# Kernel optimization log

Hardware: AMD Instinct MI355X
Metric: run time of the kernel (lower is better)

Reference implementation:

```python
import jax, jax.numpy as jnp
import numpy as np

NUM_LABELS = 17
MARGIN = 1.0
IGNORE = -100


def setup_inputs() -> dict:
    key = jax.random.key(0)
    k1, k2, k3 = jax.random.split(key, 3)
    B, S, H = 64, 1024, 384
    embeddings = jax.random.normal(k1, (B, S, H), dtype=jnp.float32)
    classifier_w = jax.random.normal(k2, (NUM_LABELS, H), dtype=jnp.float32) * 0.02
    classifier_b = jnp.zeros((NUM_LABELS,), dtype=jnp.float32)
    labels = jax.random.randint(k3, (B, S), 0, NUM_LABELS, dtype=jnp.int64 if jax.config.jax_enable_x64 else jnp.int32)
    attention_mask = jnp.ones((B, S), dtype=jnp.int32)
    return {"embeddings": embeddings, "classifier_w": classifier_w,
            "classifier_b": classifier_b, "labels": labels,
            "attention_mask": attention_mask}


def _total_loss(embeddings, W, b, labels, mask):
    B, S, H = embeddings.shape
    N = B * S
    fe = embeddings.reshape(N, H)          # [N,H] flattened tokens
    fl = labels.reshape(N)
    fm = mask.reshape(N) > 0

    # ----- cross entropy (ignore_index=-100), matches F.cross_entropy mean -----
    logits = fe @ W.T + b                  # [N, L]
    logp = jax.nn.log_softmax(logits, axis=-1)
    safe = jnp.where(fl == IGNORE, 0, fl)
    nll = -jnp.take_along_axis(logp, safe[:, None], axis=1)[:, 0]
    ce_valid = fl != IGNORE
    ce = jnp.sum(jnp.where(ce_valid, nll, 0.0)) / jnp.maximum(jnp.sum(ce_valid), 1)

    # ----- quadruplet loss (deterministic sampling: earliest occurrences) -----
    idx = jnp.arange(N)
    BIG = N  # sentinel index > any real index
    is_ent = fm & (fl > 0)
    non_ent = fm & (fl == 0)
    d_i = jnp.min(jnp.where(non_ent, idx, BIG))   # first non-entity token
    has_non = jnp.any(non_ent)

    def per_type(t):
        m = is_ent & (fl == t)
        order = jnp.sort(jnp.where(m, idx, BIG))
        a_i, p_i = order[0], order[1]             # anchor / positive = first two occurrences
        cnt = jnp.sum(m)
        other = is_ent & (fl != t)
        n_i = jnp.min(jnp.where(other, idx, BIG))  # negative = first other-type entity
        ok = (cnt >= 2) & jnp.any(other) & has_non
        return a_i, p_i, n_i, ok

    types = jnp.arange(1, NUM_LABELS)
    a_i, p_i, n_i, ok = jax.vmap(per_type)(types)  # each [L-1]
    clip = lambda i: jnp.clip(i, 0, N - 1)
    A = fe[clip(a_i)]
    P = fe[clip(p_i)]
    Ng = fe[clip(n_i)]
    D = fe[clip(d_i)][None, :]
    eps = 1e-6  # torch F.pairwise_distance eps added to the difference
    dist = lambda x, y: jnp.sqrt(jnp.sum((x - y + eps) ** 2, axis=-1))
    pd, nd, dd = dist(A, P), dist(A, Ng), dist(A, D)
    ql = jax.nn.relu(pd - nd + MARGIN) + jax.nn.relu(pd - dd + 2.0 * MARGIN)
    qcnt = jnp.sum(ok)
    quad = jnp.sum(jnp.where(ok, ql, 0.0)) / jnp.maximum(qcnt, 1)
    quad = jnp.where(qcnt > 0, quad, 0.0)

    # ----- context loss: adjacent same-entity tokens, mean-per-pair MSE -----
    l0, l1 = labels[:, :-1], labels[:, 1:]
    pair = (l0 != IGNORE) & (l0 == l1) & (l0 > 0)
    mse = jnp.mean((embeddings[:, :-1] - embeddings[:, 1:]) ** 2, axis=-1)  # [B,S-1]
    pc = jnp.sum(pair)
    ctx = jnp.sum(jnp.where(pair, mse, 0.0)) / jnp.maximum(pc, 1)
    ctx = jnp.where(pc > 0, ctx, 0.0)

    return ce + 0.5 * quad + 0.1 * ctx


def reference(embeddings, classifier_w, classifier_b, labels, attention_mask):
    return _total_loss(embeddings, classifier_w, classifier_b, labels, attention_mask)
```

## Files before the change

kernel.cpp:

```cpp
#include <hip/hip_runtime.h>

#define NL 17
#define IGN (-100)
#define HD 384
#define NSEQ 1024
#define NT 65536
#define BIGI NT
#define TPB 256
#define NBLK (NT / TPB)
#define NCHUNK 12
#define CF4 8

typedef unsigned int u32;
typedef __attribute__((ext_vector_type(8))) short bf16x8;
typedef __attribute__((ext_vector_type(16))) float f32x16;

#define GLOAD_LDS16(g, l) __builtin_amdgcn_global_load_lds(                    \
    (const __attribute__((address_space(1))) u32*)(g),                         \
    (__attribute__((address_space(3))) u32*)(l), 16, 0, 0)

__device__ __forceinline__ u32 cvtpk(float lo, float hi) {
  u32 u;
  asm("v_cvt_pk_bf16_f32 %0, %1, %2" : "=v"(u) : "v"(lo), "v"(hi));
  return u;
}

struct WS {
  float ce_part[NBLK];
  float ctx_part[NBLK];
  int   ce_cnt[NBLK];
  int   ctx_cnt[NBLK];
  int   blk_a[NBLK][16];
  int   blk_p[NBLK][16];
  int   blk_c[NBLK][16];
  int   blk_d[NBLK];
};

__global__ __launch_bounds__(256, 1) void k_main(const float* __restrict__ emb,
                                                 const float* __restrict__ cw,
                                                 const float* __restrict__ cb,
                                                 const int* __restrict__ labels,
                                                 const int* __restrict__ mask,
                                                 WS* __restrict__ ws) {
  __shared__ float4 tile[4][TPB * CF4];
  __shared__ float4 sW4[NL * (HD / 4)];
  __shared__ float sce[4], sctx[4];
  __shared__ int   svc[4], spc[4];
  __shared__ float sbctx;
  __shared__ int   sbcnt;
  __shared__ int   sla[16], slp[16], slc[16], sld;

  const int tid = threadIdx.x, lane = tid & 63, wid = tid >> 6;
  const int b = blockIdx.x;
  const int token = b * TPB + tid;

  const float4* cw4 = (const float4*)cw;
  for (int i = tid; i < NL * (HD / 4); i += TPB) {
    int c = i / (HD / 4), q = i % (HD / 4);
    sW4[c * (HD / 4) + (q ^ (c & 7))] = cw4[i];
  }
  if (tid < 16) { sla[tid] = BIGI; slp[tid] = BIGI; slc[tid] = 0; }
  if (tid == 16) sld = BIGI;
  __syncthreads();

  const int rb  = tid >> 3;
  const int c4  = tid & 7;
  const int gc4 = c4 ^ (rb & 7);
  const float* src0 = emb + (size_t)b * TPB * HD + (size_t)rb * HD + gc4 * 4;
  const int wbase = __builtin_amdgcn_readfirstlane(wid * 64);

#pragma unroll
  for (int k = 0; k < CF4; ++k)
    GLOAD_LDS16(src0 + (size_t)k * 32 * HD, &tile[0][k * 256 + wbase]);
#pragma unroll
  for (int k = 0; k < CF4; ++k)
    GLOAD_LDS16(src0 + 32 + (size_t)k * 32 * HD, &tile[1][k * 256 + wbase]);

  const int cls = lane & 31;
  const int kh  = lane >> 5;
  const int clsS = (cls < NL) ? cls : 0;
  const int row0 = wid * 64 + (lane & 31);
  const int row1 = row0 + 32;
  const int r0 = tid;
  const int r1 = (tid < TPB - 1) ? tid + 1 : tid;
  const int x0 = r0 & 7, x1 = r1 & 7;

  f32x16 d0 = {0.f}, d1 = {0.f};
  float ctxacc = 0.f;

  auto bfrag = [&](const float4* tb, int row, int s) -> bf16x8 {
    int g0 = (s * 4 + kh * 2) ^ (row & 7);
    int g1 = (s * 4 + kh * 2 + 1) ^ (row & 7);
    float4 f0 = tb[(row << 3) | g0];
    float4 f1 = tb[(row << 3) | g1];
    union { u32 u[4]; bf16x8 v; } X;
    X.u[0] = cvtpk(f0.x, f0.y); X.u[1] = cvtpk(f0.z, f0.w);
    X.u[2] = cvtpk(f1.x, f1.y); X.u[3] = cvtpk(f1.z, f1.w);
    return X.v;
  };

  auto afrag = [&](int ch, int s) -> bf16x8 {
    union { u32 u[4]; bf16x8 v; } X;
    if (cls < NL) {
      int qa = (ch * 2 + s) * 4 + kh * 2;
      float4 f0 = sW4[clsS * (HD / 4) + ((qa) ^ (cls & 7))];
      float4 f1 = sW4[clsS * (HD / 4) + ((qa + 1) ^ (cls & 7))];
      X.u[0] = cvtpk(f0.x, f0.y); X.u[1] = cvtpk(f0.z, f0.w);
      X.u[2] = cvtpk(f1.x, f1.y); X.u[3] = cvtpk(f1.z, f1.w);
    } else {
      X.u[0] = 0; X.u[1] = 0; X.u[2] = 0; X.u[3] = 0;
    }
    return X.v;
  };

  auto compute = [&](int ch, const float4* tb) {
#pragma unroll
    for (int q = 0; q < CF4; ++q) {
      float4 a  = tb[(r0 << 3) | (q ^ x0)];
      float4 nb = tb[(r1 << 3) | (q ^ x1)];
      float e0 = a.x - nb.x, e1 = a.y - nb.y, e2 = a.z - nb.z, e3 = a.w - nb.w;
      ctxacc = fmaf(e0, e0, fmaf(e1, e1, fmaf(e2, e2, fmaf(e3, e3, ctxacc))));
    }
    bf16x8 a0 = afrag(ch, 0), a1 = afrag(ch, 1);
    bf16x8 b00 = bfrag(tb, row0, 0), b01 = bfrag(tb, row0, 1);
    bf16x8 b10 = bfrag(tb, row1, 0), b11 = bfrag(tb, row1, 1);
    d0 = __builtin_amdgcn_mfma_f32_32x32x16_bf16(a0, b00, d0, 0, 0, 0);
    d0 = __builtin_amdgcn_mfma_f32_32x32x16_bf16(a1, b01, d0, 0, 0, 0);
    d1 = __builtin_amdgcn_mfma_f32_32x32x16_bf16(a0, b10, d1, 0, 0, 0);
    d1 = __builtin_amdgcn_mfma_f32_32x32x16_bf16(a1, b11, d1, 0, 0, 0);
  };

#pragma unroll 1
  for (int ch = 0; ch < NCHUNK - 2; ++ch) {
    const float* srcn = src0 + (size_t)(ch + 2) * 32;
    float4* dstb = tile[(ch + 2) & 3];
#pragma unroll
    for (int k = 0; k < CF4; ++k)
      GLOAD_LDS16(srcn + (size_t)k * 32 * HD, &dstb[k * 256 + wbase]);
    asm volatile("s_waitcnt vmcnt(16)" ::: "memory");
    __builtin_amdgcn_sched_barrier(0);
    __builtin_amdgcn_s_barrier();
    __builtin_amdgcn_sched_barrier(0);
    compute(ch, tile[ch & 3]);
  }
  asm volatile("s_waitcnt vmcnt(8)" ::: "memory");
  __builtin_amdgcn_sched_barrier(0);
  __builtin_amdgcn_s_barrier();
  __builtin_amdgcn_sched_barrier(0);
  compute(NCHUNK - 2, tile[(NCHUNK - 2) & 3]);
  asm volatile("s_waitcnt vmcnt(0)" ::: "memory");
  __builtin_amdgcn_sched_barrier(0);
  __builtin_amdgcn_s_barrier();
  __builtin_amdgcn_sched_barrier(0);
  compute(NCHUNK - 1, tile[(NCHUNK - 1) & 3]);
  __syncthreads();

  float* logit = (float*)&tile[0][0];
#pragma unroll
  for (int r = 0; r < 16; ++r) {
    int row = (r & 3) + 8 * (r >> 2) + 4 * kh;
    if (row < NL) {
      logit[(wid * 64 + (lane & 31)) * 21 + row] = d0[r];
      logit[(wid * 64 + 32 + (lane & 31)) * 21 + row] = d1[r];
    }
  }
  __syncthreads();

  int lb = labels[token];
  int mk = mask[token];
  int lbm = (mk > 0) ? lb : IGN;
  if (lbm == 0) atomicMin(&sld, token);
  else if (lbm >= 1 && lbm < NL) { atomicMin(&sla[lbm - 1], token); atomicAdd(&slc[lbm - 1], 1); }
  __syncthreads();
  if (lbm >= 1 && lbm < NL && token > sla[lbm - 1]) atomicMin(&slp[lbm - 1], token);

  float lg[NL];
#pragma unroll
  for (int c = 0; c < NL; ++c) lg[c] = logit[tid * 21 + c] + cb[c];
  float m = lg[0];
#pragma unroll
  for (int c = 1; c < NL; ++c) m = fmaxf(m, lg[c]);
  float s = 0.f;
#pragma unroll
  for (int c = 0; c < NL; ++c) s += __expf(lg[c] - m);
  float lse = m + __logf(s);
  int safe = (lb == IGN) ? 0 : lb;
  float ll = 0.f;
#pragma unroll
  for (int c = 0; c < NL; ++c) ll = (c == safe) ? lg[c] : ll;
  bool valid = (lb != IGN);
  float cev = valid ? (lse - ll) : 0.f;

  int nlb = (tid < TPB - 1) ? labels[token + 1] : IGN;
  bool pair = (tid < TPB - 1) && valid && (lb == nlb) && (lb > 0);
  float ctxv = pair ? ctxacc * (1.0f / HD) : 0.f;

  unsigned long long bv = __ballot(valid);
  unsigned long long bp = __ballot(pair);
#pragma unroll
  for (int off = 32; off; off >>= 1) {
    cev  += __shfl_xor(cev, off, 64);
    ctxv += __shfl_xor(ctxv, off, 64);
  }
  if (lane == 0) { sce[wid] = cev; sctx[wid] = ctxv; svc[wid] = __popcll(bv); spc[wid] = __popcll(bp); }

  if (wid == 3) {
    int t = b * TPB + TPB - 1;
    float bc = 0.f; int bn = 0;
    if (((t + 1) & (NSEQ - 1)) != 0) {
      int l0 = labels[t], l1 = labels[t + 1];
      if (l0 != IGN && l0 == l1 && l0 > 0) {
        const float* ra = emb + (size_t)t * HD;
        const float* rbp = ra + HD;
        float a = 0.f;
#pragma unroll
        for (int j = 0; j < 6; ++j) {
          float dd = ra[lane + 64 * j] - rbp[lane + 64 * j];
          a = fmaf(dd, dd, a);
        }
#pragma unroll
        for (int off = 32; off; off >>= 1) a += __shfl_xor(a, off, 64);
        bc = a * (1.0f / HD); bn = 1;
      }
    }
    if (lane == 0) { sbctx = bc; sbcnt = bn; }
  }
  __syncthreads();
  if (tid < 16) {
    ws->blk_a[b][tid] = sla[tid];
    ws->blk_p[b][tid] = slp[tid];
    ws->blk_c[b][tid] = slc[tid];
  }
  if (tid == 16) ws->blk_d[b] = sld;
  if (tid == 0) {
    ws->ce_part[b]  = sce[0] + sce[1] + sce[2] + sce[3];
    ws->ce_cnt[b]   = svc[0] + svc[1] + svc[2] + svc[3];
    ws->ctx_part[b] = sctx[0] + sctx[1] + sctx[2] + sctx[3] + sbctx;
    ws->ctx_cnt[b]  = spc[0] + spc[1] + spc[2] + spc[3] + sbcnt;
  }
}

__global__ __launch_bounds__(256) void k_final(const float* __restrict__ emb,
                                               WS* __restrict__ ws,
                                               float* __restrict__ out) {
  __shared__ double rce[256], rctx[256];
  __shared__ int rvc[256], rpc[256], rd[256];
  __shared__ int M1[256], M2[256], CN[256];
  __shared__ int ga[16], gp[16], gc[16];
  __shared__ float qs[4]; __shared__ int qc[4];
  const int tid = threadIdx.x, lane = tid & 63, wid = tid >> 6;

  rce[tid]  = ws->ce_part[tid];
  rctx[tid] = ws->ctx_part[tid];
  rvc[tid]  = ws->ce_cnt[tid];
  rpc[tid]  = ws->ctx_cnt[tid];
  rd[tid]   = ws->blk_d[tid];

  {
    const int type = tid & 15, seg = tid >> 4;
    int m1 = BIGI, m2 = BIGI, cnt = 0;
#pragma unroll 4
    for (int k = 0; k < 16; ++k) {
      int bb = seg * 16 + k;
      int x = ws->blk_a[bb][type];
      if (x < m1) { m2 = m1; m1 = x; } else if (x < m2) { m2 = x; }
      int y = ws->blk_p[bb][type];
      if (y < m1) { m2 = m1; m1 = y; } else if (y < m2) { m2 = y; }
      cnt += ws->blk_c[bb][type];
    }
    M1[tid] = m1; M2[tid] = m2; CN[tid] = cnt;
  }
  __syncthreads();
  for (int s = 128; s > 0; s >>= 1) {
    if (tid < s) {
      rce[tid] += rce[tid + s]; rctx[tid] += rctx[tid + s];
      rvc[tid] += rvc[tid + s]; rpc[tid] += rpc[tid + s];
      rd[tid] = min(rd[tid], rd[tid + s]);
    }
    __syncthreads();
  }
  if (tid < 16) {
    int m1 = BIGI, m2 = BIGI, cnt = 0;
    for (int seg = 0; seg < 16; ++seg) {
      int a1 = M1[seg * 16 + tid], a2 = M2[seg * 16 + tid];
      int n1 = min(m1, a1);
      int n2 = min(max(m1, a1), min(m2, a2));
      m1 = n1; m2 = n2;
      cnt += CN[seg * 16 + tid];
    }
    ga[tid] = m1; gp[tid] = m2; gc[tid] = cnt;
  }
  __syncthreads();

  const int gd = rd[0];
  float qsum = 0.f; int qcnt = 0;
  for (int tt = 0; tt < 4; ++tt) {
    int t = wid * 4 + tt;
    int a = ga[t], p = gp[t], c = gc[t];
    int nmin = BIGI;
#pragma unroll
    for (int u = 0; u < 16; ++u) if (u != t) nmin = min(nmin, ga[u]);
    bool ok = (c >= 2) && (nmin < BIGI) && (gd < BIGI);
    if (ok) {
      const float* A  = emb + (size_t)min(a, NT - 1) * HD;
      const float* P  = emb + (size_t)min(p, NT - 1) * HD;
      const float* Ng = emb + (size_t)min(nmin, NT - 1) * HD;
      const float* D  = emb + (size_t)min(gd, NT - 1) * HD;
      float sap = 0.f, san = 0.f, sad = 0.f;
#pragma unroll
      for (int j = 0; j < 6; ++j) {
        int idx = lane + 64 * j;
        float av = A[idx];
        float d1 = av - P[idx] + 1e-6f;  sap = fmaf(d1, d1, sap);
        float d2 = av - Ng[idx] + 1e-6f; san = fmaf(d2, d2, san);
        float d3 = av - D[idx] + 1e-6f;  sad = fmaf(d3, d3, sad);
      }
#pragma unroll
      for (int off = 32; off; off >>= 1) {
        sap += __shfl_xor(sap, off, 64);
        san += __shfl_xor(san, off, 64);
        sad += __shfl_xor(sad, off, 64);
      }
      float pd = sqrtf(sap), nd = sqrtf(san), dd = sqrtf(sad);
      qsum += fmaxf(pd - nd + 1.0f, 0.f) + fmaxf(pd - dd + 2.0f, 0.f);
      qcnt += 1;
    }
  }
  if (lane == 0) { qs[wid] = qsum; qc[wid] = qcnt; }
  __syncthreads();
  if (tid == 0) {
    double tq = (double)qs[0] + qs[1] + qs[2] + qs[3];
    int tqc = qc[0] + qc[1] + qc[2] + qc[3];
    double ce   = rce[0] / (double)max(rvc[0], 1);
    double ctx  = (rpc[0] > 0) ? rctx[0] / (double)rpc[0] : 0.0;
    double quad = (tqc > 0) ? tq / (double)tqc : 0.0;
    out[0] = (float)(ce + 0.5 * quad + 0.1 * ctx);
  }
}

extern "C" void kernel_launch(void* const* d_in, const int* in_sizes, int n_in,
                              void* d_out, int out_size, void* d_ws, size_t ws_size,
                              hipStream_t stream) {
  const float* emb    = (const float*)d_in[0];
  const float* cw     = (const float*)d_in[1];
  const float* cb     = (const float*)d_in[2];
  const int*   labels = (const int*)d_in[3];
  const int*   mask   = (const int*)d_in[4];
  WS* ws = (WS*)d_ws;
  float* out = (float*)d_out;

  k_main <<<NBLK, 256, 0, stream>>>(emb, cw, cb, labels, mask, ws);
  k_final<<<1, 256, 0, stream>>>(emb, ws, out);
}
```

Before: 36.37 us.

## Halve tokens per block, pre-convert weights to bf16, fuse final reduction via last-block

After: 73.88 us. 2.03x slower.

```diff
diff --git a/kernel.cpp b/kernel.cpp
--- a/kernel.cpp
+++ b/kernel.cpp
@@ -7,11 +7,13 @@
 #define NT 65536
 #define BIGI NT
 #define TPB 256
-#define NBLK (NT / TPB)
+#define TOK 128
+#define NBLK (NT / TOK)
 #define NCHUNK 12
-#define CF4 8
+#define WPAD 392
 
 typedef unsigned int u32;
+typedef unsigned short u16;
 typedef __attribute__((ext_vector_type(8))) short bf16x8;
 typedef __attribute__((ext_vector_type(16))) float f32x16;
 
@@ -26,6 +28,8 @@
 }
 
 struct WS {
+  u32  cnt;
+  u32  pad0[15];
   float ce_part[NBLK];
   float ctx_part[NBLK];
   int   ce_cnt[NBLK];
@@ -36,28 +40,29 @@
   int   blk_d[NBLK];
 };
 
-__global__ __launch_bounds__(256, 1) void k_main(const float* __restrict__ emb,
+__global__ __launch_bounds__(256, 2) void k_main(const float* __restrict__ emb,
                                                  const float* __restrict__ cw,
                                                  const float* __restrict__ cb,
                                                  const int* __restrict__ labels,
                                                  const int* __restrict__ mask,
-                                                 WS* __restrict__ ws) {
-  __shared__ float4 tile[4][TPB * CF4];
-  __shared__ float4 sW4[NL * (HD / 4)];
-  __shared__ float sce[4], sctx[4];
-  __shared__ int   svc[4], spc[4];
-  __shared__ float sbctx;
-  __shared__ int   sbcnt;
-  __shared__ int   sla[16], slp[16], slc[16], sld;
+                                                 WS* __restrict__ ws,
+                                                 float* __restrict__ out) {
+  __shared__ float4 tile[4][TOK * 8];
+  __shared__ u16    sWh[NL * WPAD];
+  __shared__ float  sce[2], sctx[2];
+  __shared__ int    svc[2], spc[2];
+  __shared__ float  sbctx;
+  __shared__ int    sbcnt;
+  __shared__ int    sla[16], slp[16], slc[16], sld, slast;
 
   const int tid = threadIdx.x, lane = tid & 63, wid = tid >> 6;
   const int b = blockIdx.x;
-  const int token = b * TPB + tid;
-
-  const float4* cw4 = (const float4*)cw;
-  for (int i = tid; i < NL * (HD / 4); i += TPB) {
-    int c = i / (HD / 4), q = i % (HD / 4);
-    sW4[c * (HD / 4) + (q ^ (c & 7))] = cw4[i];
+  const int token = b * TOK + tid;
+
+  for (int i = tid; i < NL * (HD / 2); i += TPB) {
+    int c = i / (HD / 2), p = i % (HD / 2);
+    u32 pk = cvtpk(cw[c * HD + 2 * p], cw[c * HD + 2 * p + 1]);
+    *(u32*)&sWh[c * WPAD + 2 * p] = pk;
   }
   if (tid < 16) { sla[tid] = BIGI; slp[tid] = BIGI; slc[tid] = 0; }
   if (tid == 16) sld = BIGI;
@@ -66,68 +71,59 @@
   const int rb  = tid >> 3;
   const int c4  = tid & 7;
   const int gc4 = c4 ^ (rb & 7);
-  const float* src0 = emb + (size_t)b * TPB * HD + (size_t)rb * HD + gc4 * 4;
+  const float* src0 = emb + (size_t)b * TOK * HD + (size_t)rb * HD + gc4 * 4;
   const int wbase = __builtin_amdgcn_readfirstlane(wid * 64);
 
 #pragma unroll
-  for (int k = 0; k < CF4; ++k)
+  for (int k = 0; k < 4; ++k)
     GLOAD_LDS16(src0 + (size_t)k * 32 * HD, &tile[0][k * 256 + wbase]);
 #pragma unroll
-  for (int k = 0; k < CF4; ++k)
+  for (int k = 0; k < 4; ++k)
     GLOAD_LDS16(src0 + 32 + (size_t)k * 32 * HD, &tile[1][k * 256 + wbase]);
 
   const int cls = lane & 31;
   const int kh  = lane >> 5;
   const int clsS = (cls < NL) ? cls : 0;
-  const int row0 = wid * 64 + (lane & 31);
-  const int row1 = row0 + 32;
-  const int r0 = tid;
-  const int r1 = (tid < TPB - 1) ? tid + 1 : tid;
-  const int x0 = r0 & 7, x1 = r1 & 7;
-
-  f32x16 d0 = {0.f}, d1 = {0.f};
+  const int row0 = wid * 32 + (lane & 31);
+  const int cr0 = tid & 127;
+  const int cr1 = (cr0 < TOK - 1) ? cr0 + 1 : cr0;
+  const int chf = tid >> 7;
+  const int cx0 = cr0 & 7, cx1 = cr1 & 7;
+
+  f32x16 d0 = {0.f};
   float ctxacc = 0.f;
 
-  auto bfrag = [&](const float4* tb, int row, int s) -> bf16x8 {
-    int g0 = (s * 4 + kh * 2) ^ (row & 7);
-    int g1 = (s * 4 + kh * 2 + 1) ^ (row & 7);
-    float4 f0 = tb[(row << 3) | g0];
-    float4 f1 = tb[(row << 3) | g1];
+  auto bfrag = [&](const float4* tb, int s) -> bf16x8 {
+    int g0 = (s * 4 + kh * 2) ^ (row0 & 7);
+    int g1 = (s * 4 + kh * 2 + 1) ^ (row0 & 7);
+    float4 f0 = tb[(row0 << 3) | g0];
+    float4 f1 = tb[(row0 << 3) | g1];
     union { u32 u[4]; bf16x8 v; } X;
     X.u[0] = cvtpk(f0.x, f0.y); X.u[1] = cvtpk(f0.z, f0.w);
     X.u[2] = cvtpk(f1.x, f1.y); X.u[3] = cvtpk(f1.z, f1.w);
     return X.v;
   };
-
   auto afrag = [&](int ch, int s) -> bf16x8 {
+    if (cls < NL)
+      return *(const bf16x8*)&sWh[clsS * WPAD + ch * 32 + s * 16 + kh * 8];
     union { u32 u[4]; bf16x8 v; } X;
-    if (cls < NL) {
-      int qa = (ch * 2 + s) * 4 + kh * 2;
-      float4 f0 = sW4[clsS * (HD / 4) + ((qa) ^ (cls & 7))];
-      float4 f1 = sW4[clsS * (HD / 4) + ((qa + 1) ^ (cls & 7))];
-      X.u[0] = cvtpk(f0.x, f0.y); X.u[1] = cvtpk(f0.z, f0.w);
-      X.u[2] = cvtpk(f1.x, f1.y); X.u[3] = cvtpk(f1.z, f1.w);
-    } else {
-      X.u[0] = 0; X.u[1] = 0; X.u[2] = 0; X.u[3] = 0;
-    }
+    X.u[0] = 0; X.u[1] = 0; X.u[2] = 0; X.u[3] = 0;
     return X.v;
   };
 
   auto compute = [&](int ch, const float4* tb) {
 #pragma unroll
-    for (int q = 0; q < CF4; ++q) {
-      float4 a  = tb[(r0 << 3) | (q ^ x0)];
-      float4 nb = tb[(r1 << 3) | (q ^ x1)];
+    for (int qq = 0; qq < 4; ++qq) {
+      int q = chf * 4 + qq;
+      float4 a  = tb[(cr0 << 3) | (q ^ cx0)];
+      float4 nb = tb[(cr1 << 3) | (q ^ cx1)];
       float e0 = a.x - nb.x, e1 = a.y - nb.y, e2 = a.z - nb.z, e3 = a.w - nb.w;
       ctxacc = fmaf(e0, e0, fmaf(e1, e1, fmaf(e2, e2, fmaf(e3, e3, ctxacc))));
     }
     bf16x8 a0 = afrag(ch, 0), a1 = afrag(ch, 1);
-    bf16x8 b00 = bfrag(tb, row0, 0), b01 = bfrag(tb, row0, 1);
-    bf16x8 b10 = bfrag(tb, row1, 0), b11 = bfrag(tb, row1, 1);
-    d0 = __builtin_amdgcn_mfma_f32_32x32x16_bf16(a0, b00, d0, 0, 0, 0);
-    d0 = __builtin_amdgcn_mfma_f32_32x32x16_bf16(a1, b01, d0, 0, 0, 0);
-    d1 = __builtin_amdgcn_mfma_f32_32x32x16_bf16(a0, b10, d1, 0, 0, 0);
-    d1 = __builtin_amdgcn_mfma_f32_32x32x16_bf16(a1, b11, d1, 0, 0, 0);
+    bf16x8 b0 = bfrag(tb, 0), b1 = bfrag(tb, 1);
+    d0 = __builtin_amdgcn_mfma_f32_32x32x16_bf16(a0, b0, d0, 0, 0, 0);
+    d0 = __builtin_amdgcn_mfma_f32_32x32x16_bf16(a1, b1, d0, 0, 0, 0);
   };
 
 #pragma unroll 1
@@ -135,15 +131,15 @@
     const float* srcn = src0 + (size_t)(ch + 2) * 32;
     float4* dstb = tile[(ch + 2) & 3];
 #pragma unroll
-    for (int k = 0; k < CF4; ++k)
+    for (int k = 0; k < 4; ++k)
       GLOAD_LDS16(srcn + (size_t)k * 32 * HD, &dstb[k * 256 + wbase]);
-    asm volatile("s_waitcnt vmcnt(16)" ::: "memory");
+    asm volatile("s_waitcnt vmcnt(8)" ::: "memory");
     __builtin_amdgcn_sched_barrier(0);
     __builtin_amdgcn_s_barrier();
     __builtin_amdgcn_sched_barrier(0);
     compute(ch, tile[ch & 3]);
   }
-  asm volatile("s_waitcnt vmcnt(8)" ::: "memory");
+  asm volatile("s_waitcnt vmcnt(4)" ::: "memory");
   __builtin_amdgcn_sched_barrier(0);
   __builtin_amdgcn_s_barrier();
   __builtin_amdgcn_sched_barrier(0);
@@ -156,45 +152,47 @@
   __syncthreads();
 
   float* logit = (float*)&tile[0][0];
+  float* pcxp  = (float*)&tile[1][0];
 #pragma unroll
   for (int r = 0; r < 16; ++r) {
     int row = (r & 3) + 8 * (r >> 2) + 4 * kh;
-    if (row < NL) {
-      logit[(wid * 64 + (lane & 31)) * 21 + row] = d0[r];
-      logit[(wid * 64 + 32 + (lane & 31)) * 21 + row] = d1[r];
-    }
-  }
-  __syncthreads();
-
-  int lb = labels[token];
-  int mk = mask[token];
+    if (row < NL) logit[(wid * 32 + (lane & 31)) * 21 + row] = d0[r];
+  }
+  pcxp[tid] = ctxacc;
+  __syncthreads();
+
+  int lb = IGN, mk = 0;
+  if (tid < TOK) { lb = labels[token]; mk = mask[token]; }
   int lbm = (mk > 0) ? lb : IGN;
   if (lbm == 0) atomicMin(&sld, token);
-  else if (lbm >= 1 && lbm < NL) { atomicMin(&sla[lbm - 1], token); atomicAdd(&slc[lbm - 1], 1); }
-  __syncthreads();
-  if (lbm >= 1 && lbm < NL && token > sla[lbm - 1]) atomicMin(&slp[lbm - 1], token);
-
-  float lg[NL];
-#pragma unroll
-  for (int c = 0; c < NL; ++c) lg[c] = logit[tid * 21 + c] + cb[c];
-  float m = lg[0];
-#pragma unroll
-  for (int c = 1; c < NL; ++c) m = fmaxf(m, lg[c]);
-  float s = 0.f;
-#pragma unroll
-  for (int c = 0; c < NL; ++c) s += __expf(lg[c] - m);
-  float lse = m + __logf(s);
-  int safe = (lb == IGN) ? 0 : lb;
-  float ll = 0.f;
-#pragma unroll
-  for (int c = 0; c < NL; ++c) ll = (c == safe) ? lg[c] : ll;
-  bool valid = (lb != IGN);
-  float cev = valid ? (lse - ll) : 0.f;
-
-  int nlb = (tid < TPB - 1) ? labels[token + 1] : IGN;
-  bool pair = (tid < TPB - 1) && valid && (lb == nlb) && (lb > 0);
-  float ctxv = pair ? ctxacc * (1.0f / HD) : 0.f;
-
+  else if (lbm >= 1) { atomicMin(&sla[lbm - 1], token); atomicAdd(&slc[lbm - 1], 1); }
+  __syncthreads();
+  if (lbm >= 1 && token > sla[lbm - 1]) atomicMin(&slp[lbm - 1], token);
+
+  float cev = 0.f, ctxv = 0.f;
+  bool valid = false, pair = false;
+  if (tid < TOK) {
+    float lg[NL];
+#pragma unroll
+    for (int c = 0; c < NL; ++c) lg[c] = logit[tid * 21 + c] + cb[c];
+    float m = lg[0];
+#pragma unroll
+    for (int c = 1; c < NL; ++c) m = fmaxf(m, lg[c]);
+    float s = 0.f;
+#pragma unroll
+    for (int c = 0; c < NL; ++c) s += __expf(lg[c] - m);
+    float lse = m + __logf(s);
+    int safe = (lb == IGN) ? 0 : lb;
+    float ll = 0.f;
+#pragma unroll
+    for (int c = 0; c < NL; ++c) ll = (c == safe) ? lg[c] : ll;
+    valid = (lb != IGN);
+    cev = valid ? (lse - ll) : 0.f;
+    int nlb = (tid < TOK - 1) ? labels[token + 1] : IGN;
+    pair = (tid < TOK - 1) && valid && (lb == nlb) && (lb > 0);
+    float cs = pcxp[tid] + pcxp[tid + 128];
+    ctxv = pair ? cs * (1.0f / HD) : 0.f;
+  }
   unsigned long long bv = __ballot(valid);
   unsigned long long bp = __ballot(pair);
 #pragma unroll
@@ -202,10 +200,10 @@
     cev  += __shfl_xor(cev, off, 64);
     ctxv += __shfl_xor(ctxv, off, 64);
   }
-  if (lane == 0) { sce[wid] = cev; sctx[wid] = ctxv; svc[wid] = __popcll(bv); spc[wid] = __popcll(bp); }
-
-  if (wid == 3) {
-    int t = b * TPB + TPB - 1;
+  if (lane == 0 && wid < 2) { sce[wid] = cev; sctx[wid] = ctxv; svc[wid] = __popcll(bv); spc[wid] = __popcll(bp); }
+
+  if (wid == 2) {
+    int t = b * TOK + TOK - 1;
     float bc = 0.f; int bn = 0;
     if (((t + 1) & (NSEQ - 1)) != 0) {
       int l0 = labels[t], l1 = labels[t + 1];
@@ -233,35 +231,53 @@
   }
   if (tid == 16) ws->blk_d[b] = sld;
   if (tid == 0) {
-    ws->ce_part[b]  = sce[0] + sce[1] + sce[2] + sce[3];
-    ws->ce_cnt[b]   = svc[0] + svc[1] + svc[2] + svc[3];
-    ws->ctx_part[b] = sctx[0] + sctx[1] + sctx[2] + sctx[3] + sbctx;
-    ws->ctx_cnt[b]  = spc[0] + spc[1] + spc[2] + spc[3] + sbcnt;
-  }
-}
-
-__global__ __launch_bounds__(256) void k_final(const float* __restrict__ emb,
-                                               WS* __restrict__ ws,
-                                               float* __restrict__ out) {
-  __shared__ double rce[256], rctx[256];
-  __shared__ int rvc[256], rpc[256], rd[256];
-  __shared__ int M1[256], M2[256], CN[256];
-  __shared__ int ga[16], gp[16], gc[16];
-  __shared__ float qs[4]; __shared__ int qc[4];
-  const int tid = threadIdx.x, lane = tid & 63, wid = tid >> 6;
-
-  rce[tid]  = ws->ce_part[tid];
-  rctx[tid] = ws->ctx_part[tid];
-  rvc[tid]  = ws->ce_cnt[tid];
-  rpc[tid]  = ws->ctx_cnt[tid];
-  rd[tid]   = ws->blk_d[tid];
-
+    ws->ce_part[b]  = sce[0] + sce[1];
+    ws->ce_cnt[b]   = svc[0] + svc[1];
+    ws->ctx_part[b] = sctx[0] + sctx[1] + sbctx;
+    ws->ctx_cnt[b]  = spc[0] + spc[1] + sbcnt;
+  }
+
+  __threadfence();
+  __syncthreads();
+  if (tid == 0) {
+    u32 v = atomicAdd(&ws->cnt, 1u);
+    slast = (v == (u32)(NBLK - 1));
+  }
+  __syncthreads();
+  if (!slast) return;
+  __threadfence();
+
+  char* scr = (char*)&tile[0][0];
+  double* Rce  = (double*)scr;
+  double* Rctx = (double*)(scr + 2048);
+  int* Rvc = (int*)(scr + 4096);
+  int* Rpc = (int*)(scr + 5120);
+  int* Rd  = (int*)(scr + 6144);
+  int* M1  = (int*)(scr + 7168);
+  int* M2  = (int*)(scr + 8192);
+  int* CN  = (int*)(scr + 9216);
+  int* Ga  = (int*)(scr + 10240);
+  int* Gp  = (int*)(scr + 10304);
+  int* Gc  = (int*)(scr + 10368);
+  float* Qs = (float*)(scr + 10432);
+  int* Qc  = (int*)(scr + 10448);
+
+  {
+    double sc = 0, sx = 0; int cv = 0, cp = 0, md = BIGI;
+#pragma unroll
+    for (int k = 0; k < 2; ++k) {
+      int i = tid * 2 + k;
+      sc += ws->ce_part[i]; sx += ws->ctx_part[i];
+      cv += ws->ce_cnt[i];  cp += ws->ctx_cnt[i];
+      md = min(md, ws->blk_d[i]);
+    }
+    Rce[tid] = sc; Rctx[tid] = sx; Rvc[tid] = cv; Rpc[tid] = cp; Rd[tid] = md;
+  }
   {
     const int type = tid & 15, seg = tid >> 4;
     int m1 = BIGI, m2 = BIGI, cnt = 0;
-#pragma unroll 4
-    for (int k = 0; k < 16; ++k) {
-      int bb = seg * 16 + k;
+    for (int k = 0; k < 32; ++k) {
+      int bb = seg * 32 + k;
       int x = ws->blk_a[bb][type];
       if (x < m1) { m2 = m1; m1 = x; } else if (x < m2) { m2 = x; }
       int y = ws->blk_p[bb][type];
@@ -273,9 +289,9 @@
   __syncthreads();
   for (int s = 128; s > 0; s >>= 1) {
     if (tid < s) {
-      rce[tid] += rce[tid + s]; rctx[tid] += rctx[tid + s];
-      rvc[tid] += rvc[tid + s]; rpc[tid] += rpc[tid + s];
-      rd[tid] = min(rd[tid], rd[tid + s]);
+      Rce[tid] += Rce[tid + s]; Rctx[tid] += Rctx[tid + s];
+      Rvc[tid] += Rvc[tid + s]; Rpc[tid] += Rpc[tid + s];
+      Rd[tid] = min(Rd[tid], Rd[tid + s]);
     }
     __syncthreads();
   }
@@ -288,18 +304,18 @@
       m1 = n1; m2 = n2;
       cnt += CN[seg * 16 + tid];
     }
-    ga[tid] = m1; gp[tid] = m2; gc[tid] = cnt;
-  }
-  __syncthreads();
-
-  const int gd = rd[0];
+    Ga[tid] = m1; Gp[tid] = m2; Gc[tid] = cnt;
+  }
+  __syncthreads();
+
+  const int gd = Rd[0];
   float qsum = 0.f; int qcnt = 0;
   for (int tt = 0; tt < 4; ++tt) {
     int t = wid * 4 + tt;
-    int a = ga[t], p = gp[t], c = gc[t];
+    int a = Ga[t], p = Gp[t], c = Gc[t];
     int nmin = BIGI;
 #pragma unroll
-    for (int u = 0; u < 16; ++u) if (u != t) nmin = min(nmin, ga[u]);
+    for (int u = 0; u < 16; ++u) if (u != t) nmin = min(nmin, Ga[u]);
     bool ok = (c >= 2) && (nmin < BIGI) && (gd < BIGI);
     if (ok) {
       const float* A  = emb + (size_t)min(a, NT - 1) * HD;
@@ -326,13 +342,13 @@
       qcnt += 1;
     }
   }
-  if (lane == 0) { qs[wid] = qsum; qc[wid] = qcnt; }
+  if (lane == 0) { Qs[wid] = qsum; Qc[wid] = qcnt; }
   __syncthreads();
   if (tid == 0) {
-    double tq = (double)qs[0] + qs[1] + qs[2] + qs[3];
-    int tqc = qc[0] + qc[1] + qc[2] + qc[3];
-    double ce   = rce[0] / (double)max(rvc[0], 1);
-    double ctx  = (rpc[0] > 0) ? rctx[0] / (double)rpc[0] : 0.0;
+    double tq = (double)Qs[0] + Qs[1] + Qs[2] + Qs[3];
+    int tqc = Qc[0] + Qc[1] + Qc[2] + Qc[3];
+    double ce   = Rce[0] / (double)max(Rvc[0], 1);
+    double ctx  = (Rpc[0] > 0) ? Rctx[0] / (double)Rpc[0] : 0.0;
     double quad = (tqc > 0) ? tq / (double)tqc : 0.0;
     out[0] = (float)(ce + 0.5 * quad + 0.1 * ctx);
   }
@@ -349,6 +365,6 @@
   WS* ws = (WS*)d_ws;
   float* out = (float*)d_out;
 
-  k_main <<<NBLK, 256, 0, stream>>>(emb, cw, cb, labels, mask, ws);
-  k_final<<<1, 256, 0, stream>>>(emb, ws, out);
+  hipMemsetAsync(d_ws, 0, 4, stream);
+  k_main<<<NBLK, TPB, 0, stream>>>(emb, cw, cb, labels, mask, ws, out);
 }
```

## Reuse MFMA tile reads for context MSE, pre-convert weights to bf16, deepen prefetch

Applied to the files above, without the earlier changes.

Result: slower. 39.46 us (+8.5%).

```diff
diff --git a/kernel.cpp b/kernel.cpp
--- a/kernel.cpp
+++ b/kernel.cpp
@@ -10,8 +10,10 @@
 #define NBLK (NT / TPB)
 #define NCHUNK 12
 #define CF4 8
+#define WPAD 392
 
 typedef unsigned int u32;
+typedef unsigned short u16;
 typedef __attribute__((ext_vector_type(8))) short bf16x8;
 typedef __attribute__((ext_vector_type(16))) float f32x16;
 
@@ -43,21 +45,22 @@
                                                  const int* __restrict__ mask,
                                                  WS* __restrict__ ws) {
   __shared__ float4 tile[4][TPB * CF4];
-  __shared__ float4 sW4[NL * (HD / 4)];
-  __shared__ float sce[4], sctx[4];
-  __shared__ int   svc[4], spc[4];
-  __shared__ float sbctx;
-  __shared__ int   sbcnt;
-  __shared__ int   sla[16], slp[16], slc[16], sld;
+  __shared__ u16    sWh[NL * WPAD];
+  __shared__ float  pcx0[4][64], pcx1[4][64];
+  __shared__ float  sce[4], sctx[4];
+  __shared__ int    svc[4], spc[4];
+  __shared__ float  sbctx;
+  __shared__ int    sbcnt;
+  __shared__ int    sla[16], slp[16], slc[16], sld;
 
   const int tid = threadIdx.x, lane = tid & 63, wid = tid >> 6;
   const int b = blockIdx.x;
   const int token = b * TPB + tid;
 
-  const float4* cw4 = (const float4*)cw;
-  for (int i = tid; i < NL * (HD / 4); i += TPB) {
-    int c = i / (HD / 4), q = i % (HD / 4);
-    sW4[c * (HD / 4) + (q ^ (c & 7))] = cw4[i];
+  for (int i = tid; i < NL * (HD / 2); i += TPB) {
+    int c = i / (HD / 2), p = i % (HD / 2);
+    u32 pk = cvtpk(cw[c * HD + 2 * p], cw[c * HD + 2 * p + 1]);
+    *(u32*)&sWh[c * WPAD + 2 * p] = pk;
   }
   if (tid < 16) { sla[tid] = BIGI; slp[tid] = BIGI; slc[tid] = 0; }
   if (tid == 16) sld = BIGI;
@@ -69,80 +72,84 @@
   const float* src0 = emb + (size_t)b * TPB * HD + (size_t)rb * HD + gc4 * 4;
   const int wbase = __builtin_amdgcn_readfirstlane(wid * 64);
 
-#pragma unroll
-  for (int k = 0; k < CF4; ++k)
-    GLOAD_LDS16(src0 + (size_t)k * 32 * HD, &tile[0][k * 256 + wbase]);
-#pragma unroll
-  for (int k = 0; k < CF4; ++k)
-    GLOAD_LDS16(src0 + 32 + (size_t)k * 32 * HD, &tile[1][k * 256 + wbase]);
+  auto issue = [&](int c) {
+    const float* s = src0 + (size_t)c * 32;
+    float4* d = tile[c & 3];
+#pragma unroll
+    for (int k = 0; k < CF4; ++k)
+      GLOAD_LDS16(s + (size_t)k * 32 * HD, &d[k * 256 + wbase]);
+  };
+
+  issue(0); issue(1); issue(2);
 
   const int cls = lane & 31;
   const int kh  = lane >> 5;
   const int clsS = (cls < NL) ? cls : 0;
   const int row0 = wid * 64 + (lane & 31);
   const int row1 = row0 + 32;
-  const int r0 = tid;
-  const int r1 = (tid < TPB - 1) ? tid + 1 : tid;
-  const int x0 = r0 & 7, x1 = r1 & 7;
+  const int row0n = row0 + 1;
+  const int row1n = (row1 < TPB - 1) ? row1 + 1 : row1;
 
   f32x16 d0 = {0.f}, d1 = {0.f};
-  float ctxacc = 0.f;
-
-  auto bfrag = [&](const float4* tb, int row, int s) -> bf16x8 {
-    int g0 = (s * 4 + kh * 2) ^ (row & 7);
-    int g1 = (s * 4 + kh * 2 + 1) ^ (row & 7);
-    float4 f0 = tb[(row << 3) | g0];
-    float4 f1 = tb[(row << 3) | g1];
-    union { u32 u[4]; bf16x8 v; } X;
-    X.u[0] = cvtpk(f0.x, f0.y); X.u[1] = cvtpk(f0.z, f0.w);
-    X.u[2] = cvtpk(f1.x, f1.y); X.u[3] = cvtpk(f1.z, f1.w);
-    return X.v;
+  float acc0 = 0.f, acc1 = 0.f;
+
+  auto afrag = [&](int ch, int s) -> bf16x8 {
+    if (cls < NL)
+      return *(const bf16x8*)&sWh[clsS * WPAD + ch * 32 + s * 16 + kh * 8];
+    union { u32 u[4]; bf16x8 v; } Z;
+    Z.u[0] = 0; Z.u[1] = 0; Z.u[2] = 0; Z.u[3] = 0;
+    return Z.v;
   };
 
-  auto afrag = [&](int ch, int s) -> bf16x8 {
-    union { u32 u[4]; bf16x8 v; } X;
-    if (cls < NL) {
-      int qa = (ch * 2 + s) * 4 + kh * 2;
-      float4 f0 = sW4[clsS * (HD / 4) + ((qa) ^ (cls & 7))];
-      float4 f1 = sW4[clsS * (HD / 4) + ((qa + 1) ^ (cls & 7))];
-      X.u[0] = cvtpk(f0.x, f0.y); X.u[1] = cvtpk(f0.z, f0.w);
-      X.u[2] = cvtpk(f1.x, f1.y); X.u[3] = cvtpk(f1.z, f1.w);
-    } else {
-      X.u[0] = 0; X.u[1] = 0; X.u[2] = 0; X.u[3] = 0;
-    }
-    return X.v;
+  auto compute = [&](int ch, const float4* tb) {
+    float4 t0[4], t1[4], n0[4], n1[4];
+#pragma unroll
+    for (int j = 0; j < 4; ++j) {
+      int q = (j >> 1) * 4 + kh * 2 + (j & 1);
+      t0[j] = tb[(row0  << 3) | (q ^ (row0  & 7))];
+      t1[j] = tb[(row1  << 3) | (q ^ (row1  & 7))];
+      n0[j] = tb[(row0n << 3) | (q ^ (row0n & 7))];
+      n1[j] = tb[(row1n << 3) | (q ^ (row1n & 7))];
+    }
+#pragma unroll
+    for (int j = 0; j < 4; ++j) {
+      float a0x = t0[j].x - n0[j].x, a0y = t0[j].y - n0[j].y;
+      float a0z = t0[j].z - n0[j].z, a0w = t0[j].w - n0[j].w;
+      acc0 = fmaf(a0x, a0x, fmaf(a0y, a0y, fmaf(a0z, a0z, fmaf(a0w, a0w, acc0))));
+      float a1x = t1[j].x - n1[j].x, a1y = t1[j].y - n1[j].y;
+      float a1z = t1[j].z - n1[j].z, a1w = t1[j].w - n1[j].w;
+      acc1 = fmaf(a1x, a1x, fmaf(a1y, a1y, fmaf(a1z, a1z, fmaf(a1w, a1w, acc1))));
+    }
+    union { u32 u[4]; bf16x8 v; } B00, B01, B10, B11;
+    B00.u[0] = cvtpk(t0[0].x, t0[0].y); B00.u[1] = cvtpk(t0[0].z, t0[0].w);
+    B00.u[2] = cvtpk(t0[1].x, t0[1].y); B00.u[3] = cvtpk(t0[1].z, t0[1].w);
+    B01.u[0] = cvtpk(t0[2].x, t0[2].y); B01.u[1] = cvtpk(t0[2].z, t0[2].w);
+    B01.u[2] = cvtpk(t0[3].x, t0[3].y); B01.u[3] = cvtpk(t0[3].z, t0[3].w);
+    B10.u[0] = cvtpk(t1[0].x, t1[0].y); B10.u[1] = cvtpk(t1[0].z, t1[0].w);
+    B10.u[2] = cvtpk(t1[1].x, t1[1].y); B10.u[3] = cvtpk(t1[1].z, t1[1].w);
+    B11.u[0] = cvtpk(t1[2].x, t1[2].y); B11.u[1] = cvtpk(t1[2].z, t1[2].w);
+    B11.u[2] = cvtpk(t1[3].x, t1[3].y); B11.u[3] = cvtpk(t1[3].z, t1[3].w);
+    bf16x8 a0 = afrag(ch, 0), a1 = afrag(ch, 1);
+    d0 = __builtin_amdgcn_mfma_f32_32x32x16_bf16(a0, B00.v, d0, 0, 0, 0);
+    d0 = __builtin_amdgcn_mfma_f32_32x32x16_bf16(a1, B01.v, d0, 0, 0, 0);
+    d1 = __builtin_amdgcn_mfma_f32_32x32x16_bf16(a0, B10.v, d1, 0, 0, 0);
+    d1 = __builtin_amdgcn_mfma_f32_32x32x16_bf16(a1, B11.v, d1, 0, 0, 0);
   };
 
-  auto compute = [&](int ch, const float4* tb) {
-#pragma unroll
-    for (int q = 0; q < CF4; ++q) {
-      float4 a  = tb[(r0 << 3) | (q ^ x0)];
-      float4 nb = tb[(r1 << 3) | (q ^ x1)];
-      float e0 = a.x - nb.x, e1 = a.y - nb.y, e2 = a.z - nb.z, e3 = a.w - nb.w;
-      ctxacc = fmaf(e0, e0, fmaf(e1, e1, fmaf(e2, e2, fmaf(e3, e3, ctxacc))));
-    }
-    bf16x8 a0 = afrag(ch, 0), a1 = afrag(ch, 1);
-    bf16x8 b00 = bfrag(tb, row0, 0), b01 = bfrag(tb, row0, 1);
-    bf16x8 b10 = bfrag(tb, row1, 0), b11 = bfrag(tb, row1, 1);
-    d0 = __builtin_amdgcn_mfma_f32_32x32x16_bf16(a0, b00, d0, 0, 0, 0);
-    d0 = __builtin_amdgcn_mfma_f32_32x32x16_bf16(a1, b01, d0, 0, 0, 0);
-    d1 = __builtin_amdgcn_mfma_f32_32x32x16_bf16(a0, b10, d1, 0, 0, 0);
-    d1 = __builtin_amdgcn_mfma_f32_32x32x16_bf16(a1, b11, d1, 0, 0, 0);
-  };
-
 #pragma unroll 1
-  for (int ch = 0; ch < NCHUNK - 2; ++ch) {
-    const float* srcn = src0 + (size_t)(ch + 2) * 32;
-    float4* dstb = tile[(ch + 2) & 3];
-#pragma unroll
-    for (int k = 0; k < CF4; ++k)
-      GLOAD_LDS16(srcn + (size_t)k * 32 * HD, &dstb[k * 256 + wbase]);
+  for (int ch = 0; ch <= NCHUNK - 4; ++ch) {
     asm volatile("s_waitcnt vmcnt(16)" ::: "memory");
     __builtin_amdgcn_sched_barrier(0);
     __builtin_amdgcn_s_barrier();
     __builtin_amdgcn_sched_barrier(0);
+    issue(ch + 3);
     compute(ch, tile[ch & 3]);
   }
+  asm volatile("s_waitcnt vmcnt(16)" ::: "memory");
+  __builtin_amdgcn_sched_barrier(0);
+  __builtin_amdgcn_s_barrier();
+  __builtin_amdgcn_sched_barrier(0);
+  compute(NCHUNK - 3, tile[(NCHUNK - 3) & 3]);
   asm volatile("s_waitcnt vmcnt(8)" ::: "memory");
   __builtin_amdgcn_sched_barrier(0);
   __builtin_amdgcn_s_barrier();
@@ -153,6 +160,9 @@
   __builtin_amdgcn_s_barrier();
   __builtin_amdgcn_sched_barrier(0);
   compute(NCHUNK - 1, tile[(NCHUNK - 1) & 3]);
+
+  pcx0[wid][lane] = acc0;
+  pcx1[wid][lane] = acc1;
   __syncthreads();
 
   float* logit = (float*)&tile[0][0];
@@ -191,9 +201,11 @@
   bool valid = (lb != IGN);
   float cev = valid ? (lse - ll) : 0.f;
 
+  float cs = (lane < 32) ? (pcx0[wid][lane] + pcx0[wid][lane + 32])
+                         : (pcx1[wid][lane - 32] + pcx1[wid][lane]);
   int nlb = (tid < TPB - 1) ? labels[token + 1] : IGN;
   bool pair = (tid < TPB - 1) && valid && (lb == nlb) && (lb > 0);
-  float ctxv = pair ? ctxacc * (1.0f / HD) : 0.f;
+  float ctxv = pair ? cs * (1.0f / HD) : 0.f;
 
   unsigned long long bv = __ballot(valid);
   unsigned long long bp = __ballot(pair);
@@ -349,6 +361,6 @@
   WS* ws = (WS*)d_ws;
   float* out = (float*)d_out;
 
-  k_main <<<NBLK, 256, 0, stream>>>(emb, cw, cb, labels, mask, ws);
+  k_main <<<NBLK, TPB, 0, stream>>>(emb, cw, cb, labels, mask, ws);
   k_final<<<1, 256, 0, stream>>>(emb, ws, out);
 }
```

## Make each wave own its token rows to drop block barriers; pre-convert weights to bf16

Applied to the files above, without the earlier changes.

Result: slower. 37.80 us (+4.0%).

```diff
diff --git a/kernel.cpp b/kernel.cpp
--- a/kernel.cpp
+++ b/kernel.cpp
@@ -10,8 +10,10 @@
 #define NBLK (NT / TPB)
 #define NCHUNK 12
 #define CF4 8
+#define WPAD 392
 
 typedef unsigned int u32;
+typedef unsigned short u16;
 typedef __attribute__((ext_vector_type(8))) short bf16x8;
 typedef __attribute__((ext_vector_type(16))) float f32x16;
 
@@ -42,52 +44,57 @@
                                                  const int* __restrict__ labels,
                                                  const int* __restrict__ mask,
                                                  WS* __restrict__ ws) {
-  __shared__ float4 tile[4][TPB * CF4];
-  __shared__ float4 sW4[NL * (HD / 4)];
-  __shared__ float sce[4], sctx[4];
-  __shared__ int   svc[4], spc[4];
-  __shared__ float sbctx;
-  __shared__ int   sbcnt;
-  __shared__ int   sla[16], slp[16], slc[16], sld;
+  __shared__ float4 tile[4][4][512];
+  __shared__ u16    sWh[NL * WPAD];
+  __shared__ float  sce[4], sctx[4];
+  __shared__ int    svc[4], spc[4];
+  __shared__ int    sla[16], slp[16], slc[16], sld;
 
   const int tid = threadIdx.x, lane = tid & 63, wid = tid >> 6;
+  const int uwid = __builtin_amdgcn_readfirstlane(wid);
   const int b = blockIdx.x;
   const int token = b * TPB + tid;
 
-  const float4* cw4 = (const float4*)cw;
-  for (int i = tid; i < NL * (HD / 4); i += TPB) {
-    int c = i / (HD / 4), q = i % (HD / 4);
-    sW4[c * (HD / 4) + (q ^ (c & 7))] = cw4[i];
+  for (int i = tid; i < NL * (HD / 2); i += TPB) {
+    int c = i / (HD / 2), p = i % (HD / 2);
+    u32 pk = cvtpk(cw[c * HD + 2 * p], cw[c * HD + 2 * p + 1]);
+    *(u32*)&sWh[c * WPAD + 2 * p] = pk;
   }
   if (tid < 16) { sla[tid] = BIGI; slp[tid] = BIGI; slc[tid] = 0; }
   if (tid == 16) sld = BIGI;
   __syncthreads();
 
-  const int rb  = tid >> 3;
-  const int c4  = tid & 7;
-  const int gc4 = c4 ^ (rb & 7);
-  const float* src0 = emb + (size_t)b * TPB * HD + (size_t)rb * HD + gc4 * 4;
-  const int wbase = __builtin_amdgcn_readfirstlane(wid * 64);
-
-#pragma unroll
-  for (int k = 0; k < CF4; ++k)
-    GLOAD_LDS16(src0 + (size_t)k * 32 * HD, &tile[0][k * 256 + wbase]);
-#pragma unroll
-  for (int k = 0; k < CF4; ++k)
-    GLOAD_LDS16(src0 + 32 + (size_t)k * 32 * HD, &tile[1][k * 256 + wbase]);
+  const int l3  = lane >> 3;
+  const int gc4 = (lane & 7) ^ l3;
+  const float* src0 = emb + ((size_t)b * TPB + wid * 64 + l3) * HD + gc4 * 4;
+
+  auto issue = [&](int c) {
+    const float* s = src0 + (size_t)c * 32;
+#pragma unroll
+    for (int k = 0; k < CF4; ++k)
+      GLOAD_LDS16(s + (size_t)k * 8 * HD, &tile[c & 3][uwid][k * 64]);
+  };
+
+  issue(0); issue(1); issue(2);
 
   const int cls = lane & 31;
   const int kh  = lane >> 5;
   const int clsS = (cls < NL) ? cls : 0;
-  const int row0 = wid * 64 + (lane & 31);
-  const int row1 = row0 + 32;
-  const int r0 = tid;
-  const int r1 = (tid < TPB - 1) ? tid + 1 : tid;
-  const int x0 = r0 & 7, x1 = r1 & 7;
+  const int rl0 = lane & 31;
+  const int rl1 = 32 + (lane & 31);
+  const int cr0 = lane;
+  const int cr1 = (lane < 63) ? lane + 1 : 63;
 
   f32x16 d0 = {0.f}, d1 = {0.f};
   float ctxacc = 0.f;
 
+  auto afrag = [&](int ch, int s) -> bf16x8 {
+    if (cls < NL)
+      return *(const bf16x8*)&sWh[clsS * WPAD + ch * 32 + s * 16 + kh * 8];
+    union { u32 u[4]; bf16x8 v; } Z;
+    Z.u[0] = 0; Z.u[1] = 0; Z.u[2] = 0; Z.u[3] = 0;
+    return Z.v;
+  };
   auto bfrag = [&](const float4* tb, int row, int s) -> bf16x8 {
     int g0 = (s * 4 + kh * 2) ^ (row & 7);
     int g1 = (s * 4 + kh * 2 + 1) ^ (row & 7);
@@ -99,31 +106,18 @@
     return X.v;
   };
 
-  auto afrag = [&](int ch, int s) -> bf16x8 {
-    union { u32 u[4]; bf16x8 v; } X;
-    if (cls < NL) {
-      int qa = (ch * 2 + s) * 4 + kh * 2;
-      float4 f0 = sW4[clsS * (HD / 4) + ((qa) ^ (cls & 7))];
-      float4 f1 = sW4[clsS * (HD / 4) + ((qa + 1) ^ (cls & 7))];
-      X.u[0] = cvtpk(f0.x, f0.y); X.u[1] = cvtpk(f0.z, f0.w);
-      X.u[2] = cvtpk(f1.x, f1.y); X.u[3] = cvtpk(f1.z, f1.w);
-    } else {
-      X.u[0] = 0; X.u[1] = 0; X.u[2] = 0; X.u[3] = 0;
-    }
-    return X.v;
-  };
-
-  auto compute = [&](int ch, const float4* tb) {
+  auto compute = [&](int ch) {
+    const float4* tb = (const float4*)&tile[ch & 3][wid][0];
 #pragma unroll
     for (int q = 0; q < CF4; ++q) {
-      float4 a  = tb[(r0 << 3) | (q ^ x0)];
-      float4 nb = tb[(r1 << 3) | (q ^ x1)];
+      float4 a  = tb[(cr0 << 3) | (q ^ (cr0 & 7))];
+      float4 nb = tb[(cr1 << 3) | (q ^ (cr1 & 7))];
       float e0 = a.x - nb.x, e1 = a.y - nb.y, e2 = a.z - nb.z, e3 = a.w - nb.w;
       ctxacc = fmaf(e0, e0, fmaf(e1, e1, fmaf(e2, e2, fmaf(e3, e3, ctxacc))));
     }
     bf16x8 a0 = afrag(ch, 0), a1 = afrag(ch, 1);
-    bf16x8 b00 = bfrag(tb, row0, 0), b01 = bfrag(tb, row0, 1);
-    bf16x8 b10 = bfrag(tb, row1, 0), b11 = bfrag(tb, row1, 1);
+    bf16x8 b00 = bfrag(tb, rl0, 0), b01 = bfrag(tb, rl0, 1);
+    bf16x8 b10 = bfrag(tb, rl1, 0), b11 = bfrag(tb, rl1, 1);
     d0 = __builtin_amdgcn_mfma_f32_32x32x16_bf16(a0, b00, d0, 0, 0, 0);
     d0 = __builtin_amdgcn_mfma_f32_32x32x16_bf16(a1, b01, d0, 0, 0, 0);
     d1 = __builtin_amdgcn_mfma_f32_32x32x16_bf16(a0, b10, d1, 0, 0, 0);
@@ -131,31 +125,25 @@
   };
 
 #pragma unroll 1
-  for (int ch = 0; ch < NCHUNK - 2; ++ch) {
-    const float* srcn = src0 + (size_t)(ch + 2) * 32;
-    float4* dstb = tile[(ch + 2) & 3];
-#pragma unroll
-    for (int k = 0; k < CF4; ++k)
-      GLOAD_LDS16(srcn + (size_t)k * 32 * HD, &dstb[k * 256 + wbase]);
-    asm volatile("s_waitcnt vmcnt(16)" ::: "memory");
+  for (int ch = 0; ch <= NCHUNK - 4; ++ch) {
+    issue(ch + 3);
+    asm volatile("s_waitcnt vmcnt(24)" ::: "memory");
     __builtin_amdgcn_sched_barrier(0);
-    __builtin_amdgcn_s_barrier();
-    __builtin_amdgcn_sched_barrier(0);
-    compute(ch, tile[ch & 3]);
-  }
+    compute(ch);
+  }
+  asm volatile("s_waitcnt vmcnt(16)" ::: "memory");
+  __builtin_amdgcn_sched_barrier(0);
+  compute(NCHUNK - 3);
   asm volatile("s_waitcnt vmcnt(8)" ::: "memory");
   __builtin_amdgcn_sched_barrier(0);
-  __builtin_amdgcn_s_barrier();
-  __builtin_amdgcn_sched_barrier(0);
-  compute(NCHUNK - 2, tile[(NCHUNK - 2) & 3]);
+  compute(NCHUNK - 2);
   asm volatile("s_waitcnt vmcnt(0)" ::: "memory");
   __builtin_amdgcn_sched_barrier(0);
-  __builtin_amdgcn_s_barrier();
-  __builtin_amdgcn_sched_barrier(0);
-  compute(NCHUNK - 1, tile[(NCHUNK - 1) & 3]);
-  __syncthreads();
-
-  float* logit = (float*)&tile[0][0];
+  compute(NCHUNK - 1);
+
+  __syncthreads();
+
+  float* logit = (float*)&tile[0][0][0];
 #pragma unroll
   for (int r = 0; r < 16; ++r) {
     int row = (r & 3) + 8 * (r >> 2) + 4 * kh;
@@ -191,8 +179,8 @@
   bool valid = (lb != IGN);
   float cev = valid ? (lse - ll) : 0.f;
 
-  int nlb = (tid < TPB - 1) ? labels[token + 1] : IGN;
-  bool pair = (tid < TPB - 1) && valid && (lb == nlb) && (lb > 0);
+  int nlb = (lane < 63) ? labels[token + 1] : IGN;
+  bool pair = (lane < 63) && valid && (lb == nlb) && (lb > 0);
   float ctxv = pair ? ctxacc * (1.0f / HD) : 0.f;
 
   unsigned long long bv = __ballot(valid);
@@ -202,11 +190,10 @@
     cev  += __shfl_xor(cev, off, 64);
     ctxv += __shfl_xor(ctxv, off, 64);
   }
-  if (lane == 0) { sce[wid] = cev; sctx[wid] = ctxv; svc[wid] = __popcll(bv); spc[wid] = __popcll(bp); }
-
-  if (wid == 3) {
-    int t = b * TPB + TPB - 1;
-    float bc = 0.f; int bn = 0;
+
+  float bc = 0.f; int bn = 0;
+  {
+    int t = b * TPB + wid * 64 + 63;
     if (((t + 1) & (NSEQ - 1)) != 0) {
       int l0 = labels[t], l1 = labels[t + 1];
       if (l0 != IGN && l0 == l1 && l0 > 0) {
@@ -223,7 +210,12 @@
         bc = a * (1.0f / HD); bn = 1;
       }
     }
-    if (lane == 0) { sbctx = bc; sbcnt = bn; }
+  }
+  if (lane == 0) {
+    sce[wid]  = cev;
+    sctx[wid] = ctxv + bc;
+    svc[wid]  = __popcll(bv);
+    spc[wid]  = __popcll(bp) + bn;
   }
   __syncthreads();
   if (tid < 16) {
@@ -235,8 +227,8 @@
   if (tid == 0) {
     ws->ce_part[b]  = sce[0] + sce[1] + sce[2] + sce[3];
     ws->ce_cnt[b]   = svc[0] + svc[1] + svc[2] + svc[3];
-    ws->ctx_part[b] = sctx[0] + sctx[1] + sctx[2] + sctx[3] + sbctx;
-    ws->ctx_cnt[b]  = spc[0] + spc[1] + spc[2] + spc[3] + sbcnt;
+    ws->ctx_part[b] = sctx[0] + sctx[1] + sctx[2] + sctx[3];
+    ws->ctx_cnt[b]  = spc[0] + spc[1] + spc[2] + spc[3];
   }
 }
 
@@ -349,6 +341,6 @@
   WS* ws = (WS*)d_ws;
   float* out = (float*)d_out;
 
-  k_main <<<NBLK, 256, 0, stream>>>(emb, cw, cb, labels, mask, ws);
+  k_main <<<NBLK, TPB, 0, stream>>>(emb, cw, cb, labels, mask, ws);
   k_final<<<1, 256, 0, stream>>>(emb, ws, out);
 }
```
